# Kernel tuning notes

Measured on AMD Instinct MI355X. Metric: run time of the kernel, lower is better.

Reference implementation:

```python
import jax, jax.numpy as jnp
import numpy as np

IH, IW = 32, 32
HEADS = 8
DIM_HEAD = 32
INNER = HEADS * DIM_HEAD  # 256
INP = 256
OUP = 256
SCALE = DIM_HEAD ** -0.5


def _relative_index(ih, iw):
    # Reproduce the torch buffer computation (meshgrid indexing='ij').
    yy, xx = np.meshgrid(np.arange(ih), np.arange(iw), indexing='ij')
    coords = np.stack([yy.ravel(), xx.ravel()])            # [2, n]
    rel = coords[:, :, None] - coords[:, None, :]          # [2, n, n]
    rel[0] += ih - 1
    rel[1] += iw - 1
    rel[0] *= 2 * iw - 1
    idx = rel.sum(0).ravel()                               # [n*n]
    return jnp.asarray(idx, dtype=jnp.int32)


def setup_inputs() -> dict:
    key = jax.random.key(0)
    k1, k2, k3, k4 = jax.random.split(key, 4)
    B, N = 16, IH * IW
    x = jax.random.normal(k1, (B, N, INP), dtype=jnp.float32)
    # Parameters (stored as [in, out] so forward is x @ W).
    W_qkv = jax.random.normal(k2, (INP, 3 * INNER), dtype=jnp.float32) * 0.02
    W_out = jax.random.normal(k3, (INNER, OUP), dtype=jnp.float32) * 0.02
    b_out = jnp.zeros((OUP,), dtype=jnp.float32)
    bias_table = jax.random.normal(k4, ((2 * IH - 1) * (2 * IW - 1), HEADS), dtype=jnp.float32) * 0.02
    rel_index = _relative_index(IH, IW)
    return {"x": x, "W_qkv": W_qkv, "W_out": W_out, "b_out": b_out,
            "bias_table": bias_table, "rel_index": rel_index}


def reference(x, W_qkv, W_out, b_out, bias_table, rel_index):
    B, N, _ = x.shape
    qkv = x @ W_qkv                                        # [B, N, 3*inner]
    q, k, v = jnp.split(qkv, 3, axis=-1)
    def to_heads(t):  # b n (h d) -> b h n d
        return t.reshape(B, N, HEADS, DIM_HEAD).transpose(0, 2, 1, 3)
    q, k, v = to_heads(q), to_heads(k), to_heads(v)
    dots = jnp.einsum('bhnd,bhmd->bhnm', q, k) * SCALE     # [B, H, N, N]
    # Gather relative position bias: [n*n, heads] -> [1, heads, n, n]
    rel_bias = bias_table[rel_index].reshape(N, N, HEADS).transpose(2, 0, 1)
    dots = dots + rel_bias[None]
    attn = jax.nn.softmax(dots, axis=-1)
    out = jnp.einsum('bhnm,bhmd->bhnd', attn, v)           # [B, H, N, D]
    out = out.transpose(0, 2, 1, 3).reshape(B, N, INNER)   # b n (h d)
    return out @ W_out + b_out
```

## Files before the change

kernel.cpp:

```cpp
#include <hip/hip_runtime.h>
#include <stdint.h>
#include <stddef.h>


typedef _Float16 f16;
typedef __attribute__((ext_vector_type(8))) _Float16 half8;
typedef __attribute__((ext_vector_type(4))) _Float16 half4;
typedef __attribute__((ext_vector_type(4))) float f32x4;

#define MFMA16(a, b, c) __builtin_amdgcn_mfma_f32_16x16x32_f16((a), (b), (c), 0, 0, 0)

__global__ __launch_bounds__(256) void prep_kernel(
    const float* __restrict__ x,
    const float* __restrict__ W_qkv, const float* __restrict__ W_out,
    const float* __restrict__ bias_table, const int* __restrict__ rel_index,
    f16* __restrict__ Wtq, f16* __restrict__ Wto, f16* __restrict__ biasC,
    f16* __restrict__ xh)
{
  (void)rel_index;
  const float kLog2e = 1.4426950408889634f;
  const float kScale = 0.17677669529663687f * kLog2e;
  int tid = blockIdx.x * 256 + threadIdx.x;
  if (tid < 24576) {
    int c = tid >> 5;
    int k8 = (tid & 31) << 3;
    float s = (c < 256) ? kScale : 1.0f;
    f16* dst = Wtq + c * 256 + k8;
#pragma unroll
    for (int j = 0; j < 8; ++j)
      dst[j] = (f16)(W_qkv[(k8 + j) * 768 + c] * s);
  } else if (tid < 32768) {
    int t = tid - 24576;
    int c = t >> 5;
    int k8 = (t & 31) << 3;
    f16* dst = Wto + c * 256 + k8;
#pragma unroll
    for (int j = 0; j < 8; ++j)
      dst[j] = (f16)W_out[(k8 + j) * 256 + c];
  } else if (tid < 97280) {
    int t = tid - 32768;
    int e = t * 8;
    int h = e / 64512;
    int r = e - h * 64512;
    int dy = r >> 10;
    int xi = (r >> 5) & 31;
    int xj0 = r & 31;
    int base = dy * 63 + xi + 31;
    f16* dst = biasC + e;
#pragma unroll
    for (int j = 0; j < 8; ++j)
      dst[j] = (f16)(bias_table[(base - (xj0 + j)) * 8 + h] * kLog2e);
  } else {
    int t = tid - 97280;
    const float* src = x + (size_t)t * 8;
    f16* dst = xh + (size_t)t * 8;
#pragma unroll
    for (int j = 0; j < 8; ++j) dst[j] = (f16)src[j];
  }
}

__global__ __launch_bounds__(256, 4) void qkv_kernel(
    const f16* __restrict__ xh, const f16* __restrict__ Wt,
    f16* __restrict__ Qh, f16* __restrict__ Kh, f16* __restrict__ Vt)
{
  __shared__ f16 Bs[64 * 256];
  int mt = blockIdx.x, nt = blockIdx.y;
  int tid = threadIdx.x;
  int wave = tid >> 6, lane = tid & 63;
  int g = lane >> 4, q16 = lane & 15;
  int cbase = nt * 64;
  char* BsB = (char*)Bs;
  const f16* WtG = Wt + (size_t)cbase * 256;
#pragma unroll
  for (int i = 0; i < 8; ++i) {
    int c = i * 256 + tid;
    int row = c >> 5;
    int colb = (c & 31) << 4;
    half8 v = *(const half8*)(WtG + c * 8);
    *(half8*)(BsB + row * 512 + (colb ^ ((row & 7) << 4))) = v;
  }
  __syncthreads();

  int rbase = mt * 256 + wave * 64;
  const f16* xr0 = xh + (size_t)(rbase + q16) * 256 + g * 8;
  f32x4 acc[4][4] = {};
#pragma unroll 2
  for (int kc = 0; kc < 8; ++kc) {
    half8 bf[4];
#pragma unroll
    for (int cf = 0; cf < 4; ++cf) {
      int row = cf * 16 + q16;
      int colb = kc * 64 + g * 16;
      bf[cf] = *(const half8*)(BsB + row * 512 + (colb ^ ((row & 7) << 4)));
    }
#pragma unroll
    for (int mf = 0; mf < 4; ++mf) {
      half8 af = *(const half8*)(xr0 + (size_t)(mf * 16) * 256 + kc * 32);
#pragma unroll
      for (int cf = 0; cf < 4; ++cf)
        acc[mf][cf] = MFMA16(af, bf[cf], acc[mf][cf]);
    }
  }

#pragma unroll
  for (int mf = 0; mf < 4; ++mf) {
#pragma unroll
    for (int cf = 0; cf < 4; ++cf) {
      int c = cbase + cf * 16 + q16;
      int which = c >> 8, h = (c >> 5) & 7, d = c & 31;
      int m0 = rbase + mf * 16 + g * 4;
      int b = m0 >> 10, n0 = m0 & 1023;
      size_t bh = (size_t)(b * 8 + h);
      if (which == 2) {
        half4 vv;
#pragma unroll
        for (int r = 0; r < 4; ++r) vv[r] = (f16)acc[mf][cf][r];
        *(half4*)(Vt + (((bh << 5) | d) << 10) + n0) = vv;
      } else {
        f16* base = (which == 0) ? Qh : Kh;
#pragma unroll
        for (int r = 0; r < 4; ++r)
          base[((bh << 10) | (n0 + r)) * 32 + d] = (f16)acc[mf][cf][r];
      }
    }
  }
}

__global__ __launch_bounds__(256) void attn_kernel(
    const f16* __restrict__ Qh, const f16* __restrict__ Kh,
    const f16* __restrict__ Vt, const f16* __restrict__ biasC,
    f16* __restrict__ Oh)
{
  int bid = blockIdx.x;
  int h = bid & 7;
  int rest = bid >> 3;
  int qt = rest & 3;
  int b = rest >> 2;
  int wave = threadIdx.x >> 6, lane = threadIdx.x & 63;
  int g = lane >> 4, q16 = lane & 15;
  int bh = b * 8 + h;
  int qbase = qt * 256 + wave * 64;
  const f16* Qb = Qh + ((size_t)bh << 15);
  const f16* Kb = Kh + ((size_t)bh << 15);
  const f16* Vb = Vt + ((size_t)bh << 15);

  half8 qf0 = *(const half8*)(Qb + (size_t)(qbase +  0 + q16) * 32 + g * 8);
  half8 qf1 = *(const half8*)(Qb + (size_t)(qbase + 16 + q16) * 32 + g * 8);
  half8 qf2 = *(const half8*)(Qb + (size_t)(qbase + 32 + q16) * 32 + g * 8);
  half8 qf3 = *(const half8*)(Qb + (size_t)(qbase + 48 + q16) * 32 + g * 8);

  int kr0 = ((q16 >> 2) << 3) | (q16 & 3);
  const f16* Kp0 = Kb + kr0 * 32 + g * 8;
  const f16* Kp1 = Kp0 + 4 * 32;
  const f16* Vp0 = Vb + (size_t)q16 * 1024 + g * 8;
  const f16* Vp1 = Vb + (size_t)(16 + q16) * 1024 + g * 8;
  int yi0 = qbase >> 5;
  const f16* Bp = biasC + ((((h * 63 + yi0 + 31) * 32 + q16) << 5) + g * 8);

  f32x4 o0a = {0.f,0.f,0.f,0.f}, o1a = {0.f,0.f,0.f,0.f};
  f32x4 o0b = {0.f,0.f,0.f,0.f}, o1b = {0.f,0.f,0.f,0.f};
  f32x4 o0c = {0.f,0.f,0.f,0.f}, o1c = {0.f,0.f,0.f,0.f};
  f32x4 o0d = {0.f,0.f,0.f,0.f}, o1d = {0.f,0.f,0.f,0.f};
  float lsa = 0.f, lsb = 0.f, lsc = 0.f, lsd = 0.f;

#define FRAG_BODY(QF, K0, K1, V0, V1, BB, O0, O1, LS)                        \
  {                                                                          \
    f32x4 c0, c1;                                                            \
    _Pragma("unroll") for (int r = 0; r < 4; ++r) {                          \
      c0[r] = (float)BB[r]; c1[r] = (float)BB[4 + r];                        \
    }                                                                        \
    f32x4 s0 = MFMA16(K0, QF, c0);                                           \
    f32x4 s1 = MFMA16(K1, QF, c1);                                           \
    float p[8];                                                              \
    _Pragma("unroll") for (int r = 0; r < 4; ++r) {                          \
      p[r]     = __builtin_amdgcn_exp2f(s0[r]);                              \
      p[4 + r] = __builtin_amdgcn_exp2f(s1[r]);                              \
    }                                                                        \
    half8 pf;                                                                \
    _Pragma("unroll") for (int i = 0; i < 8; ++i) {                          \
      LS += p[i]; pf[i] = (f16)p[i];                                         \
    }                                                                        \
    O0 = MFMA16(V0, pf, O0);                                                 \
    O1 = MFMA16(V1, pf, O1);                                                 \
  }

  half8 kA0 = *(const half8*)Kp0;
  half8 kA1 = *(const half8*)Kp1;
  half8 vA0 = *(const half8*)Vp0;
  half8 vA1 = *(const half8*)Vp1;
  half8 bA0 = *(const half8*)(Bp);
  half8 bA1 = *(const half8*)(Bp + 512);
  half8 bA2 = *(const half8*)(Bp + 1024);
  half8 bA3 = *(const half8*)(Bp + 1536);

  for (int kt = 0; kt < 31; ++kt) {
    size_t ko = (size_t)(kt + 1) * 1024;
    int    co = (kt + 1) * 32;
    const f16* Bn = Bp - ko;
    half8 kB0 = *(const half8*)(Kp0 + ko);
    half8 kB1 = *(const half8*)(Kp1 + ko);
    half8 vB0 = *(const half8*)(Vp0 + co);
    half8 vB1 = *(const half8*)(Vp1 + co);
    half8 bB0 = *(const half8*)(Bn);
    half8 bB1 = *(const half8*)(Bn + 512);
    half8 bB2 = *(const half8*)(Bn + 1024);
    half8 bB3 = *(const half8*)(Bn + 1536);
    FRAG_BODY(qf0, kA0, kA1, vA0, vA1, bA0, o0a, o1a, lsa);
    FRAG_BODY(qf1, kA0, kA1, vA0, vA1, bA1, o0b, o1b, lsb);
    FRAG_BODY(qf2, kA0, kA1, vA0, vA1, bA2, o0c, o1c, lsc);
    FRAG_BODY(qf3, kA0, kA1, vA0, vA1, bA3, o0d, o1d, lsd);
    kA0 = kB0; kA1 = kB1; vA0 = vB0; vA1 = vB1;
    bA0 = bB0; bA1 = bB1; bA2 = bB2; bA3 = bB3;
  }
  FRAG_BODY(qf0, kA0, kA1, vA0, vA1, bA0, o0a, o1a, lsa);
  FRAG_BODY(qf1, kA0, kA1, vA0, vA1, bA1, o0b, o1b, lsb);
  FRAG_BODY(qf2, kA0, kA1, vA0, vA1, bA2, o0c, o1c, lsc);
  FRAG_BODY(qf3, kA0, kA1, vA0, vA1, bA3, o0d, o1d, lsd);
#undef FRAG_BODY

#define FRAG_OUT(O0, O1, LS, FOFF)                                           \
  {                                                                          \
    float l = LS;                                                            \
    l += __shfl_xor(l, 16);                                                  \
    l += __shfl_xor(l, 32);                                                  \
    float invl = 1.0f / l;                                                   \
    f16* op = Oh + (((size_t)bh << 10) + qbase + (FOFF) + q16) * 32;         \
    half4 w0, w1;                                                            \
    _Pragma("unroll") for (int r = 0; r < 4; ++r) {                          \
      w0[r] = (f16)(O0[r] * invl); w1[r] = (f16)(O1[r] * invl);              \
    }                                                                        \
    *(half4*)(op + g * 4) = w0;                                              \
    *(half4*)(op + 16 + g * 4) = w1;                                         \
  }
  FRAG_OUT(o0a, o1a, lsa, 0);
  FRAG_OUT(o0b, o1b, lsb, 16);
  FRAG_OUT(o0c, o1c, lsc, 32);
  FRAG_OUT(o0d, o1d, lsd, 48);
#undef FRAG_OUT
}

__global__ __launch_bounds__(256, 4) void out_kernel(
    const f16* __restrict__ Oh, const f16* __restrict__ Wto,
    const float* __restrict__ b_out, float* __restrict__ out)
{
  __shared__ f16 Bs[64 * 256];
  int mt = blockIdx.x, nt = blockIdx.y;
  int tid = threadIdx.x;
  int wave = tid >> 6, lane = tid & 63;
  int g = lane >> 4, q16 = lane & 15;
  int cbase = nt * 64;
  char* BsB = (char*)Bs;
  const f16* WtG = Wto + (size_t)cbase * 256;
#pragma unroll
  for (int i = 0; i < 8; ++i) {
    int c = i * 256 + tid;
    int row = c >> 5;
    int colb = (c & 31) << 4;
    half8 v = *(const half8*)(WtG + c * 8);
    *(half8*)(BsB + row * 512 + (colb ^ ((row & 7) << 4))) = v;
  }
  __syncthreads();

  int rbase = mt * 256 + wave * 64;
  int b = rbase >> 10;
  int nb = rbase & 1023;
  f32x4 acc[4][4] = {};
#pragma unroll 2
  for (int kc = 0; kc < 8; ++kc) {
    half8 bf[4];
#pragma unroll
    for (int cf = 0; cf < 4; ++cf) {
      int row = cf * 16 + q16;
      int colb = kc * 64 + g * 16;
      bf[cf] = *(const half8*)(BsB + row * 512 + (colb ^ ((row & 7) << 4)));
    }
#pragma unroll
    for (int mf = 0; mf < 4; ++mf) {
      int n = nb + mf * 16 + q16;
      half8 af = *(const half8*)(Oh + ((((size_t)(b * 8 + kc)) << 10) | n) * 32 + g * 8);
#pragma unroll
      for (int cf = 0; cf < 4; ++cf)
        acc[mf][cf] = MFMA16(af, bf[cf], acc[mf][cf]);
    }
  }

#pragma unroll
  for (int mf = 0; mf < 4; ++mf) {
#pragma unroll
    for (int cf = 0; cf < 4; ++cf) {
      int c = cbase + cf * 16 + q16;
      float bias = b_out[c];
#pragma unroll
      for (int r = 0; r < 4; ++r) {
        int mm = rbase + mf * 16 + g * 4 + r;
        out[(size_t)mm * 256 + c] = acc[mf][cf][r] + bias;
      }
    }
  }
}

extern "C" void kernel_launch(void* const* d_in, const int* in_sizes, int n_in,
                              void* d_out, int out_size, void* d_ws, size_t ws_size,
                              hipStream_t stream) {
  (void)in_sizes; (void)n_in; (void)out_size; (void)ws_size;
  const float* x        = (const float*)d_in[0];
  const float* W_qkv    = (const float*)d_in[1];
  const float* W_out    = (const float*)d_in[2];
  const float* b_out    = (const float*)d_in[3];
  const float* bias_tab = (const float*)d_in[4];
  const int*   rel_idx  = (const int*)d_in[5];
  float* out = (float*)d_out;
  char* ws = (char*)d_ws;

  f16* Qh     = (f16*)(ws);
  f16* Kh     = (f16*)(ws + (size_t)(8u  << 20));
  f16* Vt     = (f16*)(ws + (size_t)(16u << 20));
  f16* biasC  = (f16*)(ws + (size_t)(24u << 20));
  f16* xh     = (f16*)(ws + (size_t)(40u << 20));
  f16* Oh     = (f16*)(ws + (size_t)(40u << 20));
  f16* Wtq    = (f16*)(ws + (size_t)(48u << 20));
  f16* Wto    = (f16*)(ws + (size_t)(48u << 20) + 768 * 256 * 2);

  hipLaunchKernelGGL(prep_kernel, dim3(2428), dim3(256), 0, stream,
                     x, W_qkv, W_out, bias_tab, rel_idx, Wtq, Wto, biasC, xh);
  hipLaunchKernelGGL(qkv_kernel, dim3(64, 12), dim3(256), 0, stream,
                     xh, Wtq, Qh, Kh, Vt);
  hipLaunchKernelGGL(attn_kernel, dim3(512), dim3(256), 0, stream,
                     Qh, Kh, Vt, biasC, Oh);
  hipLaunchKernelGGL(out_kernel, dim3(64, 4), dim3(256), 0, stream,
                     Oh, Wto, b_out, out);
}
```

Before: 81.83 us.

## Split attention into finer query tiles, keep bias in fp32, pack exp conversions

The attention grid doubles to 1024 blocks, each wave handling 32 query rows instead of 64, with a min-blocks launch bound of 4 to raise occupancy. The precomputed relative-position bias is now stored in fp32, so it feeds the MFMA accumulator directly with no per-element fp16-to-fp32 conversion. Exponentials are packed with cvt_pkrtz, and row sums use fdot2 on the packed fp16 values. The cost is that each K/V fragment load is amortized over fewer query fragments, and the bias buffer doubles in bytes read.

Measured after the change: 141.0 us. 1.72x slower.

```diff
diff --git a/kernel.cpp b/kernel.cpp
--- a/kernel.cpp
+++ b/kernel.cpp
@@ -6,6 +6,7 @@
 typedef _Float16 f16;
 typedef __attribute__((ext_vector_type(8))) _Float16 half8;
 typedef __attribute__((ext_vector_type(4))) _Float16 half4;
+typedef __attribute__((ext_vector_type(2))) __fp16 fp16x2;
 typedef __attribute__((ext_vector_type(4))) float f32x4;
 
 #define MFMA16(a, b, c) __builtin_amdgcn_mfma_f32_16x16x32_f16((a), (b), (c), 0, 0, 0)
@@ -14,7 +15,7 @@
     const float* __restrict__ x,
     const float* __restrict__ W_qkv, const float* __restrict__ W_out,
     const float* __restrict__ bias_table, const int* __restrict__ rel_index,
-    f16* __restrict__ Wtq, f16* __restrict__ Wto, f16* __restrict__ biasC,
+    f16* __restrict__ Wtq, f16* __restrict__ Wto, float* __restrict__ biasC,
     f16* __restrict__ xh)
 {
   (void)rel_index;
@@ -46,10 +47,10 @@
     int xi = (r >> 5) & 31;
     int xj0 = r & 31;
     int base = dy * 63 + xi + 31;
-    f16* dst = biasC + e;
+    float* dst = biasC + e;
 #pragma unroll
     for (int j = 0; j < 8; ++j)
-      dst[j] = (f16)(bias_table[(base - (xj0 + j)) * 8 + h] * kLog2e);
+      dst[j] = bias_table[(base - (xj0 + j)) * 8 + h] * kLog2e;
   } else {
     int t = tid - 97280;
     const float* src = x + (size_t)t * 8;
@@ -126,28 +127,26 @@
   }
 }
 
-__global__ __launch_bounds__(256) void attn_kernel(
+__global__ __launch_bounds__(256, 4) void attn_kernel(
     const f16* __restrict__ Qh, const f16* __restrict__ Kh,
-    const f16* __restrict__ Vt, const f16* __restrict__ biasC,
+    const f16* __restrict__ Vt, const float* __restrict__ biasC,
     f16* __restrict__ Oh)
 {
   int bid = blockIdx.x;
   int h = bid & 7;
   int rest = bid >> 3;
-  int qt = rest & 3;
-  int b = rest >> 2;
+  int qt = rest & 7;
+  int b = rest >> 3;
   int wave = threadIdx.x >> 6, lane = threadIdx.x & 63;
   int g = lane >> 4, q16 = lane & 15;
   int bh = b * 8 + h;
-  int qbase = qt * 256 + wave * 64;
+  int qbase = qt * 128 + wave * 32;
   const f16* Qb = Qh + ((size_t)bh << 15);
   const f16* Kb = Kh + ((size_t)bh << 15);
   const f16* Vb = Vt + ((size_t)bh << 15);
 
   half8 qf0 = *(const half8*)(Qb + (size_t)(qbase +  0 + q16) * 32 + g * 8);
   half8 qf1 = *(const half8*)(Qb + (size_t)(qbase + 16 + q16) * 32 + g * 8);
-  half8 qf2 = *(const half8*)(Qb + (size_t)(qbase + 32 + q16) * 32 + g * 8);
-  half8 qf3 = *(const half8*)(Qb + (size_t)(qbase + 48 + q16) * 32 + g * 8);
 
   int kr0 = ((q16 >> 2) << 3) | (q16 & 3);
   const f16* Kp0 = Kb + kr0 * 32 + g * 8;
@@ -155,72 +154,79 @@
   const f16* Vp0 = Vb + (size_t)q16 * 1024 + g * 8;
   const f16* Vp1 = Vb + (size_t)(16 + q16) * 1024 + g * 8;
   int yi0 = qbase >> 5;
-  const f16* Bp = biasC + ((((h * 63 + yi0 + 31) * 32 + q16) << 5) + g * 8);
+  const float* Bp = biasC + (((h * 63 + yi0 + 31) * 32 + q16) << 5) + g * 8;
 
   f32x4 o0a = {0.f,0.f,0.f,0.f}, o1a = {0.f,0.f,0.f,0.f};
   f32x4 o0b = {0.f,0.f,0.f,0.f}, o1b = {0.f,0.f,0.f,0.f};
-  f32x4 o0c = {0.f,0.f,0.f,0.f}, o1c = {0.f,0.f,0.f,0.f};
-  f32x4 o0d = {0.f,0.f,0.f,0.f}, o1d = {0.f,0.f,0.f,0.f};
-  float lsa = 0.f, lsb = 0.f, lsc = 0.f, lsd = 0.f;
-
-#define FRAG_BODY(QF, K0, K1, V0, V1, BB, O0, O1, LS)                        \
+  float lsa0 = 0.f, lsa1 = 0.f, lsb0 = 0.f, lsb1 = 0.f;
+  const fp16x2 one2 = {(__fp16)1.0f, (__fp16)1.0f};
+  (void)one2;
+
+#if __has_builtin(__builtin_amdgcn_fdot2)
+#define LSUM(LS0, LS1, PU)                                                   \
+    LS0 = __builtin_amdgcn_fdot2(PU.h2[0], one2, LS0, false);                \
+    LS0 = __builtin_amdgcn_fdot2(PU.h2[1], one2, LS0, false);                \
+    LS1 = __builtin_amdgcn_fdot2(PU.h2[2], one2, LS1, false);                \
+    LS1 = __builtin_amdgcn_fdot2(PU.h2[3], one2, LS1, false);
+#else
+#define LSUM(LS0, LS1, PU)                                                   \
+    _Pragma("unroll") for (int i = 0; i < 4; ++i) {                          \
+      LS0 += (float)PU.h8[i]; LS1 += (float)PU.h8[4 + i];                    \
+    }
+#endif
+
+#define FRAG_BODY(QF, K0, K1, V0, V1, BLO, BHI, O0, O1, LS0, LS1)            \
   {                                                                          \
-    f32x4 c0, c1;                                                            \
-    _Pragma("unroll") for (int r = 0; r < 4; ++r) {                          \
-      c0[r] = (float)BB[r]; c1[r] = (float)BB[4 + r];                        \
-    }                                                                        \
-    f32x4 s0 = MFMA16(K0, QF, c0);                                           \
-    f32x4 s1 = MFMA16(K1, QF, c1);                                           \
-    float p[8];                                                              \
-    _Pragma("unroll") for (int r = 0; r < 4; ++r) {                          \
-      p[r]     = __builtin_amdgcn_exp2f(s0[r]);                              \
-      p[4 + r] = __builtin_amdgcn_exp2f(s1[r]);                              \
-    }                                                                        \
-    half8 pf;                                                                \
-    _Pragma("unroll") for (int i = 0; i < 8; ++i) {                          \
-      LS += p[i]; pf[i] = (f16)p[i];                                         \
-    }                                                                        \
-    O0 = MFMA16(V0, pf, O0);                                                 \
-    O1 = MFMA16(V1, pf, O1);                                                 \
+    f32x4 s0 = MFMA16(K0, QF, BLO);        \
+    f32x4 s1 = MFMA16(K1, QF, BHI);                                          \
+    union { fp16x2 h2[4]; half8 h8; } pu;                                    \
+    pu.h2[0] = __builtin_amdgcn_cvt_pkrtz(                                   \
+        __builtin_amdgcn_exp2f(s0[0]), __builtin_amdgcn_exp2f(s0[1]));       \
+    pu.h2[1] = __builtin_amdgcn_cvt_pkrtz(                                   \
+        __builtin_amdgcn_exp2f(s0[2]), __builtin_amdgcn_exp2f(s0[3]));       \
+    pu.h2[2] = __builtin_amdgcn_cvt_pkrtz(                                   \
+        __builtin_amdgcn_exp2f(s1[0]), __builtin_amdgcn_exp2f(s1[1]));       \
+    pu.h2[3] = __builtin_amdgcn_cvt_pkrtz(                                   \
+        __builtin_amdgcn_exp2f(s1[2]), __builtin_amdgcn_exp2f(s1[3]));       \
+    LSUM(LS0, LS1, pu)                                                       \
+    O0 = MFMA16(V0, pu.h8, O0);                                              \
+    O1 = MFMA16(V1, pu.h8, O1);                                              \
   }
 
   half8 kA0 = *(const half8*)Kp0;
   half8 kA1 = *(const half8*)Kp1;
   half8 vA0 = *(const half8*)Vp0;
   half8 vA1 = *(const half8*)Vp1;
-  half8 bA0 = *(const half8*)(Bp);
-  half8 bA1 = *(const half8*)(Bp + 512);
-  half8 bA2 = *(const half8*)(Bp + 1024);
-  half8 bA3 = *(const half8*)(Bp + 1536);
+  f32x4 bA0lo = *(const f32x4*)(Bp);
+  f32x4 bA0hi = *(const f32x4*)(Bp + 4);
+  f32x4 bA1lo = *(const f32x4*)(Bp + 512);
+  f32x4 bA1hi = *(const f32x4*)(Bp + 516);
 
   for (int kt = 0; kt < 31; ++kt) {
     size_t ko = (size_t)(kt + 1) * 1024;
     int    co = (kt + 1) * 32;
-    const f16* Bn = Bp - ko;
+    const float* Bn = Bp - ko;
     half8 kB0 = *(const half8*)(Kp0 + ko);
     half8 kB1 = *(const half8*)(Kp1 + ko);
     half8 vB0 = *(const half8*)(Vp0 + co);
     half8 vB1 = *(const half8*)(Vp1 + co);
-    half8 bB0 = *(const half8*)(Bn);
-    half8 bB1 = *(const half8*)(Bn + 512);
-    half8 bB2 = *(const half8*)(Bn + 1024);
-    half8 bB3 = *(const half8*)(Bn + 1536);
-    FRAG_BODY(qf0, kA0, kA1, vA0, vA1, bA0, o0a, o1a, lsa);
-    FRAG_BODY(qf1, kA0, kA1, vA0, vA1, bA1, o0b, o1b, lsb);
-    FRAG_BODY(qf2, kA0, kA1, vA0, vA1, bA2, o0c, o1c, lsc);
-    FRAG_BODY(qf3, kA0, kA1, vA0, vA1, bA3, o0d, o1d, lsd);
+    f32x4 bB0lo = *(const f32x4*)(Bn);
+    f32x4 bB0hi = *(const f32x4*)(Bn + 4);
+    f32x4 bB1lo = *(const f32x4*)(Bn + 512);
+    f32x4 bB1hi = *(const f32x4*)(Bn + 516);
+    FRAG_BODY(qf0, kA0, kA1, vA0, vA1, bA0lo, bA0hi, o0a, o1a, lsa0, lsa1);
+    FRAG_BODY(qf1, kA0, kA1, vA0, vA1, bA1lo, bA1hi, o0b, o1b, lsb0, lsb1);
     kA0 = kB0; kA1 = kB1; vA0 = vB0; vA1 = vB1;
-    bA0 = bB0; bA1 = bB1; bA2 = bB2; bA3 = bB3;
-  }
-  FRAG_BODY(qf0, kA0, kA1, vA0, vA1, bA0, o0a, o1a, lsa);
-  FRAG_BODY(qf1, kA0, kA1, vA0, vA1, bA1, o0b, o1b, lsb);
-  FRAG_BODY(qf2, kA0, kA1, vA0, vA1, bA2, o0c, o1c, lsc);
-  FRAG_BODY(qf3, kA0, kA1, vA0, vA1, bA3, o0d, o1d, lsd);
+    bA0lo = bB0lo; bA0hi = bB0hi; bA1lo = bB1lo; bA1hi = bB1hi;
+  }
+  FRAG_BODY(qf0, kA0, kA1, vA0, vA1, bA0lo, bA0hi, o0a, o1a, lsa0, lsa1);
+  FRAG_BODY(qf1, kA0, kA1, vA0, vA1, bA1lo, bA1hi, o0b, o1b, lsb0, lsb1);
 #undef FRAG_BODY
-
-#define FRAG_OUT(O0, O1, LS, FOFF)                                           \
+#undef LSUM
+
+#define FRAG_OUT(O0, O1, LS0, LS1, FOFF)                                     \
   {                                                                          \
-    float l = LS;                                                            \
+    float l = LS0 + LS1;                                                     \
     l += __shfl_xor(l, 16);                                                  \
     l += __shfl_xor(l, 32);                                                  \
     float invl = 1.0f / l;                                                   \
@@ -232,10 +238,8 @@
     *(half4*)(op + g * 4) = w0;                                              \
     *(half4*)(op + 16 + g * 4) = w1;                                         \
   }
-  FRAG_OUT(o0a, o1a, lsa, 0);
-  FRAG_OUT(o0b, o1b, lsb, 16);
-  FRAG_OUT(o0c, o1c, lsc, 32);
-  FRAG_OUT(o0d, o1d, lsd, 48);
+  FRAG_OUT(o0a, o1a, lsa0, lsa1, 0);
+  FRAG_OUT(o0b, o1b, lsb0, lsb1, 16);
 #undef FRAG_OUT
 }
 
@@ -312,20 +316,20 @@
   float* out = (float*)d_out;
   char* ws = (char*)d_ws;
 
-  f16* Qh     = (f16*)(ws);
-  f16* Kh     = (f16*)(ws + (size_t)(8u  << 20));
-  f16* Vt     = (f16*)(ws + (size_t)(16u << 20));
-  f16* biasC  = (f16*)(ws + (size_t)(24u << 20));
-  f16* xh     = (f16*)(ws + (size_t)(40u << 20));
-  f16* Oh     = (f16*)(ws + (size_t)(40u << 20));
-  f16* Wtq    = (f16*)(ws + (size_t)(48u << 20));
-  f16* Wto    = (f16*)(ws + (size_t)(48u << 20) + 768 * 256 * 2);
+  f16*   Qh    = (f16*)(ws);
+  f16*   Kh    = (f16*)(ws + (size_t)(8u  << 20));
+  f16*   Vt    = (f16*)(ws + (size_t)(16u << 20));
+  float* biasC = (float*)(ws + (size_t)(24u << 20));
+  f16*   xh    = (f16*)(ws + (size_t)(40u << 20));
+  f16*   Oh    = (f16*)(ws + (size_t)(40u << 20));
+  f16*   Wtq   = (f16*)(ws + (size_t)(48u << 20));
+  f16*   Wto   = (f16*)(ws + (size_t)(48u << 20) + 768 * 256 * 2);
 
   hipLaunchKernelGGL(prep_kernel, dim3(2428), dim3(256), 0, stream,
                      x, W_qkv, W_out, bias_tab, rel_idx, Wtq, Wto, biasC, xh);
   hipLaunchKernelGGL(qkv_kernel, dim3(64, 12), dim3(256), 0, stream,
                      xh, Wtq, Qh, Kh, Vt);
-  hipLaunchKernelGGL(attn_kernel, dim3(512), dim3(256), 0, stream,
+  hipLaunchKernelGGL(attn_kernel, dim3(1024), dim3(256), 0, stream,
                      Qh, Kh, Vt, biasC, Oh);
   hipLaunchKernelGGL(out_kernel, dim3(64, 4), dim3(256), 0, stream,
                      Oh, Wto, b_out, out);
```
